# Kernel optimization log

Measured on AMD Instinct MI355X. Metric: run time of the kernel, lower is better.

Reference implementation:

```python
import jax, jax.numpy as jnp
import numpy as np

B, M, N, L = 8, 384, 1536, 20  # batch, checks (detectors), error mechanisms, BP layers
ROW_W = 8  # check-node degree of sparse parity-check matrix H


def setup_inputs() -> dict:
    key = jax.random.key(0)
    ks = jax.random.split(key, 10)
    # Sparse binary check matrix: each row has exactly ROW_W ones (LDPC-like DEM).
    rng = np.random.default_rng(0)
    H_np = np.zeros((M, N), np.float32)
    for i in range(M):
        H_np[i, rng.choice(N, ROW_W, replace=False)] = 1.0
    H = jnp.asarray(H_np)
    llrs = jax.random.uniform(ks[0], (N,), minval=0.5, maxval=2.0)
    syndromes = jax.random.randint(ks[1], (B, M, 1), 0, 2).astype(jnp.float32)
    errors = jax.random.randint(ks[2], (B, N), 0, 2).astype(jnp.float32)
    # Per-layer learned weights (damped so 20 BP iterations stay numerically stable).
    weights_de = jax.random.uniform(ks[3], (L, M, N), minval=0.1, maxval=0.25)
    weights_llr = jax.random.uniform(ks[4], (L, N), minval=0.5, maxval=1.0)
    marg_weights_de = jax.random.uniform(ks[5], (M, N), minval=0.5, maxval=1.0)
    marg_weights_llr = jax.random.uniform(ks[6], (N,), minval=0.5, maxval=1.0)
    residual_weights = jax.random.uniform(ks[7], (L,), minval=0.0, maxval=0.1)
    rhos = jnp.ones((L,), jnp.float32) / L  # init: ones normalized by layers
    return dict(syndromes=syndromes, errors=errors, H=H, llrs=llrs,
                weights_de=weights_de, weights_llr=weights_llr,
                marg_weights_de=marg_weights_de, marg_weights_llr=marg_weights_llr,
                residual_weights=residual_weights, rhos=rhos)


def reference(syndromes, errors, H, llrs, weights_de, weights_llr,
              marg_weights_de, marg_weights_llr, residual_weights, rhos):
    sign = (1.0 - 2.0 * syndromes) * H          # (B,M,N): (-1)^syndrome masked by H
    one_minus_e = 1.0 - errors                  # (B,N)

    def step(msg_dn, per_layer):
        w_de, w_llr, res_w, rho = per_layer
        # --- error (variable) node update ---
        base = H * (llrs * w_llr)                                     # (M,N)
        msg_en = (base + jnp.sum(msg_dn * w_de, axis=1, keepdims=True)) * H - msg_dn
        # --- detector (check) node update: tanh-product with self-exclusion by division ---
        d = jnp.tanh(msg_en * 0.5)
        d = jnp.where(d == 0.0, 1.0, d)
        p = jnp.prod(d, axis=2, keepdims=True)                        # (B,M,1)
        msg_dn_new = 2.0 * jnp.arctanh(p / d) * sign + res_w * msg_dn
        # --- marginals (beliefs) + per-layer loss ---
        beliefs = jnp.sum(msg_dn_new * marg_weights_de, axis=1) + llrs * marg_weights_llr  # (B,N)
        loss_b = jnp.sum(jax.nn.softplus(beliefs) - one_minus_e * beliefs, axis=1) * rho   # (B,)
        return msg_dn_new, loss_b

    msg0 = jnp.zeros((syndromes.shape[0], H.shape[0], H.shape[1]), jnp.float32)
    _, losses = jax.lax.scan(step, msg0, (weights_de, weights_llr, residual_weights, rhos))
    return jnp.sum(losses) / syndromes.shape[0]  # scalar mean-over-batch loss
```

## Files before the change

### kernel.cpp

```cpp
#include <hip/hip_runtime.h>
#include <math.h>

#define MB 8
#define MM 384
#define NN 1536
#define LL 20
#define RW 8
#define HE 4
#define NE (MM*RW)
#define NT 768
#define VP 12

__global__ __launch_bounds__(256) void setup_kernel(
    const float* __restrict__ H,
    const float* __restrict__ llrs,
    const float* __restrict__ w_llr,
    const float* __restrict__ w_de,
    const float* __restrict__ marg_de,
    int*   __restrict__ col_idx,
    float* __restrict__ marg_e,
    float* __restrict__ base_e,
    float* __restrict__ wde_e,
    float* __restrict__ out) {
    const int m = blockIdx.x;
    const int t = threadIdx.x;
    const int w = t >> 6, lane = t & 63;
    __shared__ int s_qcol[4][RW];
    __shared__ int s_qcnt[4];
    __shared__ int s_col[RW];

    const float* row = H + (size_t)m * NN;
    int count = 0;
    for (int c0 = w * 384; c0 < (w + 1) * 384; c0 += 64) {
        float v = row[c0 + lane];
        unsigned long long mask = __ballot(v != 0.0f);
        if (v != 0.0f) {
            int pos = count + (int)__popcll(mask & ((1ull << lane) - 1ull));
            if (pos < RW) s_qcol[w][pos] = c0 + lane;
        }
        count += (int)__popcll(mask);
    }
    if (lane == 0) s_qcnt[w] = (count < RW) ? count : RW;
    __syncthreads();
    if (t == 0) {
        int off = 0;
        for (int q = 0; q < 4; ++q)
            for (int i = 0; i < s_qcnt[q]; ++i) {
                if (off < RW) s_col[off] = s_qcol[q][i];
                ++off;
            }
    }
    __syncthreads();

    if (t < RW) {
        int c = s_col[t];
        col_idx[m * RW + t] = c;
        marg_e[m * RW + t]  = marg_de[m * NN + c];
    }
    if (m == 0 && t == 0) out[0] = 0.0f;

    for (int idx = t; idx < LL * RW; idx += 256) {
        int l = idx >> 3;
        int k = idx & 7;
        int c = s_col[k];
        base_e[l * NE + m * RW + k] = llrs[c] * w_llr[l * NN + c];
        wde_e [l * NE + m * RW + k] = w_de[(size_t)l * MM * NN + (size_t)m * NN + c];
    }
}

__global__ __launch_bounds__(NT) void bp_kernel(
    const float* __restrict__ synd,
    const float* __restrict__ errors,
    const float* __restrict__ llrs,
    const float* __restrict__ marg_llr,
    const float* __restrict__ res_w,
    const float* __restrict__ rhos,
    const int*   __restrict__ col_idx,
    const float* __restrict__ marg_e_g,
    const float* __restrict__ base_e_g,
    const float* __restrict__ wde_e_g,
    float* __restrict__ out) {

    __shared__ float s_S[NN];
    __shared__ float s_cS[NE];
    __shared__ float s_cB[NE];
    __shared__ unsigned short s_vslot[NN*VP];
    __shared__ int   s_vdeg[NN];
    __shared__ float s_rw[LL];
    __shared__ float s_rho[LL];
    __shared__ float s_red[12];

    const int b = blockIdx.x;
    const int t = threadIdx.x;
    const int m = t >> 1;

    int col[HE];
    {
        const int4 ci = ((const int4*)col_idx)[t];
        col[0] = ci.x; col[1] = ci.y; col[2] = ci.z; col[3] = ci.w;
    }
    float msg[HE] = {0.0f, 0.0f, 0.0f, 0.0f};
    float marg[HE];
    {
        const float4 mg = ((const float4*)marg_e_g)[t];
        marg[0] = mg.x; marg[1] = mg.y; marg[2] = mg.z; marg[3] = mg.w;
    }
    const float sgn = 1.0f - 2.0f * synd[b * MM + m];

    float bias[2], omeg[2];
    #pragma unroll
    for (int i = 0; i < 2; ++i) {
        int n = t + i * NT;
        bias[i] = llrs[n] * marg_llr[n];
        omeg[i] = 1.0f - errors[b * NN + n];
        s_vdeg[n] = 0;
    }
    #pragma unroll
    for (int k = 0; k < HE; ++k) {
        s_cS[k * NT + t] = 0.0f;
        s_cB[k * NT + t] = 0.0f;
    }
    if (t < LL) { s_rw[t] = res_w[t]; s_rho[t] = rhos[t]; }
    __syncthreads();

    #pragma unroll
    for (int k = 0; k < HE; ++k) {
        int c = col[k];
        int pos = atomicAdd(&s_vdeg[c], 1);
        if (pos < VP) s_vslot[c * VP + pos] = (unsigned short)(k * NT + t);
    }
    __syncthreads();

    int deg0 = s_vdeg[t];        if (deg0 > VP) deg0 = VP;
    int deg1 = s_vdeg[t + NT];   if (deg1 > VP) deg1 = VP;
    int sl0[VP], sl1[VP];
    #pragma unroll
    for (int j = 0; j < VP; ++j) {
        sl0[j] = (j < deg0) ? (int)s_vslot[t * VP + j] : 0;
        sl1[j] = (j < deg1) ? (int)s_vslot[(t + NT) * VP + j] : 0;
    }

    float bc[HE], wS[HE], bn[HE], wn2[HE];
    {
        const float4 bp4 = ((const float4*)(base_e_g))[t];
        bc[0] = bp4.x; bc[1] = bp4.y; bc[2] = bp4.z; bc[3] = bp4.w;
        const float4 wp4 = ((const float4*)(wde_e_g + 1 * NE))[t];
        wS[0] = wp4.x; wS[1] = wp4.y; wS[2] = wp4.z; wS[3] = wp4.w;
    }

    float loss = 0.0f;
    __syncthreads();

    for (int l = 0; l < LL; ++l) {
        {
            int lb = (l + 1 < LL) ? (l + 1) : (LL - 1);
            int lw = (l + 2 < LL) ? (l + 2) : (LL - 1);
            const float4 bp4 = ((const float4*)(base_e_g + lb * NE))[t];
            bn[0]  = bp4.x; bn[1]  = bp4.y; bn[2]  = bp4.z; bn[3]  = bp4.w;
            const float4 wp4 = ((const float4*)(wde_e_g + lw * NE))[t];
            wn2[0] = wp4.x; wn2[1] = wp4.y; wn2[2] = wp4.z; wn2[3] = wp4.w;
        }

        {
            float S0 = 0.0f, S1 = 0.0f;
            float bel0 = bias[0], bel1 = bias[1];
            #pragma unroll
            for (int j = 0; j < VP; ++j) {
                if (j < deg0) { S0 += s_cS[sl0[j]]; bel0 += s_cB[sl0[j]]; }
                if (j < deg1) { S1 += s_cS[sl1[j]]; bel1 += s_cB[sl1[j]]; }
            }
            s_S[t]      = S0;
            s_S[t + NT] = S1;
            if (l > 0) {
                const float rr = s_rho[l - 1];
                float sp0 = fmaxf(bel0, 0.0f) + __logf(1.0f + __expf(-fabsf(bel0)));
                float sp1 = fmaxf(bel1, 0.0f) + __logf(1.0f + __expf(-fabsf(bel1)));
                loss += rr * ((sp0 - omeg[0] * bel0) + (sp1 - omeg[1] * bel1));
            }
        }
        __syncthreads();

        const float rw_ = s_rw[l];

        float d[HE];
        #pragma unroll
        for (int k = 0; k < HE; ++k) {
            float te = bc[k] + s_S[col[k]] - msg[k];
            float e  = __expf(te);
            float dd = 1.0f - 2.0f * __builtin_amdgcn_rcpf(e + 1.0f);
            dd = fminf(fmaxf(dd, -1.0f), 1.0f);
            if (dd == 0.0f) dd = 1.0f;
            d[k] = dd;
        }
        float p01 = d[0] * d[1], p23 = d[2] * d[3];
        float p4  = p01 * p23;
        float pot = __shfl_xor(p4, 1, 64);
        float ptot = p4 * pot;

        #pragma unroll
        for (int k = 0; k < HE; ++k) {
            float x  = ptot * __builtin_amdgcn_rcpf(d[k]);
            float r  = (1.0f + x) * __builtin_amdgcn_rcpf(1.0f - x);
            float nm = sgn * __logf(r) + rw_ * msg[k];
            msg[k] = nm;
            s_cS[k * NT + t] = nm * wS[k];
            s_cB[k * NT + t] = nm * marg[k];
        }

        #pragma unroll
        for (int k = 0; k < HE; ++k) { bc[k] = bn[k]; wS[k] = wn2[k]; }

        __syncthreads();
    }

    {
        const float rr = s_rho[LL - 1];
        float bel0 = bias[0], bel1 = bias[1];
        #pragma unroll
        for (int j = 0; j < VP; ++j) {
            if (j < deg0) bel0 += s_cB[sl0[j]];
            if (j < deg1) bel1 += s_cB[sl1[j]];
        }
        float sp0 = fmaxf(bel0, 0.0f) + __logf(1.0f + __expf(-fabsf(bel0)));
        float sp1 = fmaxf(bel1, 0.0f) + __logf(1.0f + __expf(-fabsf(bel1)));
        loss += rr * ((sp0 - omeg[0] * bel0) + (sp1 - omeg[1] * bel1));
    }

    #pragma unroll
    for (int off = 32; off > 0; off >>= 1)
        loss += __shfl_down(loss, off, 64);
    int wave = t >> 6, lane = t & 63;
    if (lane == 0) s_red[wave] = loss;
    __syncthreads();
    if (t == 0) {
        float tot = 0.0f;
        #pragma unroll
        for (int w = 0; w < 12; ++w) tot += s_red[w];
        atomicAdd(out, tot * (1.0f / (float)MB));
    }
}

extern "C" void kernel_launch(void* const* d_in, const int* in_sizes, int n_in,
                              void* d_out, int out_size, void* d_ws, size_t ws_size,
                              hipStream_t stream) {
    const float* synd     = (const float*)d_in[0];
    const float* errors   = (const float*)d_in[1];
    const float* H        = (const float*)d_in[2];
    const float* llrs     = (const float*)d_in[3];
    const float* w_de     = (const float*)d_in[4];
    const float* w_llr    = (const float*)d_in[5];
    const float* marg_de  = (const float*)d_in[6];
    const float* marg_llr = (const float*)d_in[7];
    const float* res_w    = (const float*)d_in[8];
    const float* rhos     = (const float*)d_in[9];
    float* out = (float*)d_out;

    int*   col_idx = (int*)d_ws;
    float* marg_e  = (float*)d_ws + NE;
    float* base_e  = marg_e + NE;
    float* wde_e   = base_e + LL * NE;

    setup_kernel<<<MM, 256, 0, stream>>>(H, llrs, w_llr, w_de, marg_de,
                                         col_idx, marg_e, base_e, wde_e, out);
    bp_kernel<<<MB, NT, 0, stream>>>(synd, errors, llrs, marg_llr, res_w, rhos,
                                     col_idx, marg_e, base_e, wde_e, out);
}
```

Measured before the change: 146.4 us.

## Store messages in variable-major padded slots and gather with weighted float4 dot products

Check-to-variable messages now go into a variable-major padded array of 12 slots per variable, and the weights for each slot (w_de and the marginal weights) are precomputed in the same transposed layout. The variable-node sums become contiguous float4 LDS reads plus FMAs, replacing indexed gathers through a slot table, and the in-kernel shared atomics for slot assignment move into setup via global atomics. This adds a zero-init kernel launch and larger per-layer weight loads, 24 floats per thread per layer instead of 4. It also uses more registers, which may lower occupancy at 768 threads.

```diff
diff --git a/kernel.cpp b/kernel.cpp
--- a/kernel.cpp
+++ b/kernel.cpp
@@ -10,6 +10,14 @@
 #define NE (MM*RW)
 #define NT 768
 #define VP 12
+#define VG 3
+
+__global__ void zero_kernel(float* __restrict__ p, int n, float* __restrict__ out) {
+    int i = blockIdx.x * blockDim.x + threadIdx.x;
+    int stride = gridDim.x * blockDim.x;
+    for (; i < n; i += stride) p[i] = 0.0f;
+    if (blockIdx.x == 0 && threadIdx.x == 0) out[0] = 0.0f;
+}
 
 __global__ __launch_bounds__(256) void setup_kernel(
     const float* __restrict__ H,
@@ -17,17 +25,18 @@
     const float* __restrict__ w_llr,
     const float* __restrict__ w_de,
     const float* __restrict__ marg_de,
-    int*   __restrict__ col_idx,
-    float* __restrict__ marg_e,
+    int*   __restrict__ col_pack,
     float* __restrict__ base_e,
-    float* __restrict__ wde_e,
-    float* __restrict__ out) {
+    float* __restrict__ wde_vT,
+    float* __restrict__ marg_vT,
+    int*   __restrict__ gcnt) {
     const int m = blockIdx.x;
     const int t = threadIdx.x;
     const int w = t >> 6, lane = t & 63;
     __shared__ int s_qcol[4][RW];
     __shared__ int s_qcnt[4];
     __shared__ int s_col[RW];
+    __shared__ int s_pos[RW];
 
     const float* row = H + (size_t)m * NN;
     int count = 0;
@@ -54,17 +63,22 @@
 
     if (t < RW) {
         int c = s_col[t];
-        col_idx[m * RW + t] = c;
-        marg_e[m * RW + t]  = marg_de[m * NN + c];
-    }
-    if (m == 0 && t == 0) out[0] = 0.0f;
+        int pos = atomicAdd(&gcnt[c], 1);
+        if (pos >= VP) pos = VP - 1;
+        s_pos[t] = pos;
+        col_pack[m * RW + t] = c | (pos << 16);
+        marg_vT[((pos >> 2) * NN + c) * 4 + (pos & 3)] = marg_de[m * NN + c];
+    }
+    __syncthreads();
 
     for (int idx = t; idx < LL * RW; idx += 256) {
         int l = idx >> 3;
         int k = idx & 7;
         int c = s_col[k];
+        int pos = s_pos[k];
+        wde_vT[((l * VG + (pos >> 2)) * NN + c) * 4 + (pos & 3)] =
+            w_de[(size_t)l * MM * NN + (size_t)m * NN + c];
         base_e[l * NE + m * RW + k] = llrs[c] * w_llr[l * NN + c];
-        wde_e [l * NE + m * RW + k] = w_de[(size_t)l * MM * NN + (size_t)m * NN + c];
     }
 }
 
@@ -75,17 +89,14 @@
     const float* __restrict__ marg_llr,
     const float* __restrict__ res_w,
     const float* __restrict__ rhos,
-    const int*   __restrict__ col_idx,
-    const float* __restrict__ marg_e_g,
+    const int*   __restrict__ col_pack,
     const float* __restrict__ base_e_g,
-    const float* __restrict__ wde_e_g,
+    const float* __restrict__ wde_vT,
+    const float* __restrict__ marg_vT,
     float* __restrict__ out) {
 
+    __shared__ float s_cN[NN * VP];
     __shared__ float s_S[NN];
-    __shared__ float s_cS[NE];
-    __shared__ float s_cB[NE];
-    __shared__ unsigned short s_vslot[NN*VP];
-    __shared__ int   s_vdeg[NN];
     __shared__ float s_rw[LL];
     __shared__ float s_rho[LL];
     __shared__ float s_red[12];
@@ -94,17 +105,18 @@
     const int t = threadIdx.x;
     const int m = t >> 1;
 
-    int col[HE];
+    int col[HE], esl[HE];
     {
-        const int4 ci = ((const int4*)col_idx)[t];
-        col[0] = ci.x; col[1] = ci.y; col[2] = ci.z; col[3] = ci.w;
+        const int4 cp = ((const int4*)col_pack)[t];
+        int v[HE] = {cp.x, cp.y, cp.z, cp.w};
+        #pragma unroll
+        for (int k = 0; k < HE; ++k) {
+            int c = v[k] & 0xFFFF, pos = v[k] >> 16;
+            col[k] = c;
+            esl[k] = ((pos >> 2) * NN + c) * 4 + (pos & 3);
+        }
     }
     float msg[HE] = {0.0f, 0.0f, 0.0f, 0.0f};
-    float marg[HE];
-    {
-        const float4 mg = ((const float4*)marg_e_g)[t];
-        marg[0] = mg.x; marg[1] = mg.y; marg[2] = mg.z; marg[3] = mg.w;
-    }
     const float sgn = 1.0f - 2.0f * synd[b * MM + m];
 
     float bias[2], omeg[2];
@@ -113,40 +125,34 @@
         int n = t + i * NT;
         bias[i] = llrs[n] * marg_llr[n];
         omeg[i] = 1.0f - errors[b * NN + n];
-        s_vdeg[n] = 0;
-    }
-    #pragma unroll
-    for (int k = 0; k < HE; ++k) {
-        s_cS[k * NT + t] = 0.0f;
-        s_cB[k * NT + t] = 0.0f;
-    }
+    }
+
+    float mg0[VP], mg1[VP];
+    #pragma unroll
+    for (int jg = 0; jg < VG; ++jg) {
+        float4 a = ((const float4*)marg_vT)[jg * NN + t];
+        mg0[jg*4+0] = a.x; mg0[jg*4+1] = a.y; mg0[jg*4+2] = a.z; mg0[jg*4+3] = a.w;
+        float4 c4 = ((const float4*)marg_vT)[jg * NN + t + NT];
+        mg1[jg*4+0] = c4.x; mg1[jg*4+1] = c4.y; mg1[jg*4+2] = c4.z; mg1[jg*4+3] = c4.w;
+    }
+    float wc0[VP], wc1[VP], wn0[VP], wn1[VP];
+    #pragma unroll
+    for (int jg = 0; jg < VG; ++jg) {
+        float4 a = ((const float4*)wde_vT)[jg * NN + t];
+        wc0[jg*4+0] = a.x; wc0[jg*4+1] = a.y; wc0[jg*4+2] = a.z; wc0[jg*4+3] = a.w;
+        float4 c4 = ((const float4*)wde_vT)[jg * NN + t + NT];
+        wc1[jg*4+0] = c4.x; wc1[jg*4+1] = c4.y; wc1[jg*4+2] = c4.z; wc1[jg*4+3] = c4.w;
+    }
+    float bc[HE], bn[HE];
+    {
+        const float4 bp4 = ((const float4*)base_e_g)[t];
+        bc[0] = bp4.x; bc[1] = bp4.y; bc[2] = bp4.z; bc[3] = bp4.w;
+    }
+
+    #pragma unroll
+    for (int j = 0; j < 6; ++j)
+        ((float4*)s_cN)[j * NT + t] = make_float4(0.f, 0.f, 0.f, 0.f);
     if (t < LL) { s_rw[t] = res_w[t]; s_rho[t] = rhos[t]; }
-    __syncthreads();
-
-    #pragma unroll
-    for (int k = 0; k < HE; ++k) {
-        int c = col[k];
-        int pos = atomicAdd(&s_vdeg[c], 1);
-        if (pos < VP) s_vslot[c * VP + pos] = (unsigned short)(k * NT + t);
-    }
-    __syncthreads();
-
-    int deg0 = s_vdeg[t];        if (deg0 > VP) deg0 = VP;
-    int deg1 = s_vdeg[t + NT];   if (deg1 > VP) deg1 = VP;
-    int sl0[VP], sl1[VP];
-    #pragma unroll
-    for (int j = 0; j < VP; ++j) {
-        sl0[j] = (j < deg0) ? (int)s_vslot[t * VP + j] : 0;
-        sl1[j] = (j < deg1) ? (int)s_vslot[(t + NT) * VP + j] : 0;
-    }
-
-    float bc[HE], wS[HE], bn[HE], wn2[HE];
-    {
-        const float4 bp4 = ((const float4*)(base_e_g))[t];
-        bc[0] = bp4.x; bc[1] = bp4.y; bc[2] = bp4.z; bc[3] = bp4.w;
-        const float4 wp4 = ((const float4*)(wde_e_g + 1 * NE))[t];
-        wS[0] = wp4.x; wS[1] = wp4.y; wS[2] = wp4.z; wS[3] = wp4.w;
-    }
 
     float loss = 0.0f;
     __syncthreads();
@@ -154,20 +160,27 @@
     for (int l = 0; l < LL; ++l) {
         {
             int lb = (l + 1 < LL) ? (l + 1) : (LL - 1);
-            int lw = (l + 2 < LL) ? (l + 2) : (LL - 1);
+            #pragma unroll
+            for (int jg = 0; jg < VG; ++jg) {
+                float4 a = ((const float4*)wde_vT)[(lb * VG + jg) * NN + t];
+                wn0[jg*4+0] = a.x; wn0[jg*4+1] = a.y; wn0[jg*4+2] = a.z; wn0[jg*4+3] = a.w;
+                float4 c4 = ((const float4*)wde_vT)[(lb * VG + jg) * NN + t + NT];
+                wn1[jg*4+0] = c4.x; wn1[jg*4+1] = c4.y; wn1[jg*4+2] = c4.z; wn1[jg*4+3] = c4.w;
+            }
             const float4 bp4 = ((const float4*)(base_e_g + lb * NE))[t];
-            bn[0]  = bp4.x; bn[1]  = bp4.y; bn[2]  = bp4.z; bn[3]  = bp4.w;
-            const float4 wp4 = ((const float4*)(wde_e_g + lw * NE))[t];
-            wn2[0] = wp4.x; wn2[1] = wp4.y; wn2[2] = wp4.z; wn2[3] = wp4.w;
+            bn[0] = bp4.x; bn[1] = bp4.y; bn[2] = bp4.z; bn[3] = bp4.w;
         }
 
         {
-            float S0 = 0.0f, S1 = 0.0f;
-            float bel0 = bias[0], bel1 = bias[1];
+            float S0 = 0.0f, S1 = 0.0f, bel0 = bias[0], bel1 = bias[1];
             #pragma unroll
-            for (int j = 0; j < VP; ++j) {
-                if (j < deg0) { S0 += s_cS[sl0[j]]; bel0 += s_cB[sl0[j]]; }
-                if (j < deg1) { S1 += s_cS[sl1[j]]; bel1 += s_cB[sl1[j]]; }
+            for (int jg = 0; jg < VG; ++jg) {
+                float4 a = ((const float4*)s_cN)[jg * NN + t];
+                S0   += a.x*wc0[jg*4+0] + a.y*wc0[jg*4+1] + a.z*wc0[jg*4+2] + a.w*wc0[jg*4+3];
+                bel0 += a.x*mg0[jg*4+0] + a.y*mg0[jg*4+1] + a.z*mg0[jg*4+2] + a.w*mg0[jg*4+3];
+                float4 c4 = ((const float4*)s_cN)[jg * NN + t + NT];
+                S1   += c4.x*wc1[jg*4+0] + c4.y*wc1[jg*4+1] + c4.z*wc1[jg*4+2] + c4.w*wc1[jg*4+3];
+                bel1 += c4.x*mg1[jg*4+0] + c4.y*mg1[jg*4+1] + c4.z*mg1[jg*4+2] + c4.w*mg1[jg*4+3];
             }
             s_S[t]      = S0;
             s_S[t + NT] = S1;
@@ -203,12 +216,13 @@
             float r  = (1.0f + x) * __builtin_amdgcn_rcpf(1.0f - x);
             float nm = sgn * __logf(r) + rw_ * msg[k];
             msg[k] = nm;
-            s_cS[k * NT + t] = nm * wS[k];
-            s_cB[k * NT + t] = nm * marg[k];
-        }
-
-        #pragma unroll
-        for (int k = 0; k < HE; ++k) { bc[k] = bn[k]; wS[k] = wn2[k]; }
+            s_cN[esl[k]] = nm;
+        }
+
+        #pragma unroll
+        for (int k = 0; k < HE; ++k) bc[k] = bn[k];
+        #pragma unroll
+        for (int j = 0; j < VP; ++j) { wc0[j] = wn0[j]; wc1[j] = wn1[j]; }
 
         __syncthreads();
     }
@@ -217,9 +231,11 @@
         const float rr = s_rho[LL - 1];
         float bel0 = bias[0], bel1 = bias[1];
         #pragma unroll
-        for (int j = 0; j < VP; ++j) {
-            if (j < deg0) bel0 += s_cB[sl0[j]];
-            if (j < deg1) bel1 += s_cB[sl1[j]];
+        for (int jg = 0; jg < VG; ++jg) {
+            float4 a = ((const float4*)s_cN)[jg * NN + t];
+            bel0 += a.x*mg0[jg*4+0] + a.y*mg0[jg*4+1] + a.z*mg0[jg*4+2] + a.w*mg0[jg*4+3];
+            float4 c4 = ((const float4*)s_cN)[jg * NN + t + NT];
+            bel1 += c4.x*mg1[jg*4+0] + c4.y*mg1[jg*4+1] + c4.z*mg1[jg*4+2] + c4.w*mg1[jg*4+3];
         }
         float sp0 = fmaxf(bel0, 0.0f) + __logf(1.0f + __expf(-fabsf(bel0)));
         float sp1 = fmaxf(bel1, 0.0f) + __logf(1.0f + __expf(-fabsf(bel1)));
@@ -255,13 +271,16 @@
     const float* rhos     = (const float*)d_in[9];
     float* out = (float*)d_out;
 
-    int*   col_idx = (int*)d_ws;
-    float* marg_e  = (float*)d_ws + NE;
-    float* base_e  = marg_e + NE;
-    float* wde_e   = base_e + LL * NE;
-
+    float* wde_vT  = (float*)d_ws;
+    float* marg_vT = wde_vT + (size_t)LL * VG * NN * 4;
+    int*   gcnt    = (int*)(marg_vT + VG * NN * 4);
+    float* base_e  = (float*)(gcnt + NN);
+    int*   col_pack= (int*)(base_e + (size_t)LL * NE);
+    const int nzero = LL * VG * NN * 4 + VG * NN * 4 + NN;
+
+    zero_kernel<<<512, 256, 0, stream>>>(wde_vT, nzero, out);
     setup_kernel<<<MM, 256, 0, stream>>>(H, llrs, w_llr, w_de, marg_de,
-                                         col_idx, marg_e, base_e, wde_e, out);
+                                         col_pack, base_e, wde_vT, marg_vT, gcnt);
     bp_kernel<<<MB, NT, 0, stream>>>(synd, errors, llrs, marg_llr, res_w, rhos,
-                                     col_idx, marg_e, base_e, wde_e, out);
-}
+                                     col_pack, base_e, wde_vT, marg_vT, out);
+}
```

Result: slower. 151.4 us (+3.4%).
